# Optimization experiments

Measured on AMD Instinct MI355X. Metric: run time of the kernel, lower is better.

## Reference

```python
import jax, jax.numpy as jnp
import numpy as np

B, L, D, H = 8, 2048, 1024, 16
FACTOR = 3


def setup_inputs() -> dict:
    key = jax.random.key(0)
    ks = jax.random.split(key, 11)
    s = 0.02
    mk = lambda k, shp: jax.random.normal(k, shp, dtype=jnp.float32)
    return {
        "queries": mk(ks[0], (B, L, D)),
        "keys": mk(ks[1], (B, L, D)),
        "values": mk(ks[2], (B, L, D)),
        "Wq": mk(ks[3], (D, D)) * s, "bq": jnp.zeros((D,), jnp.float32),
        "Wk": mk(ks[4], (D, D)) * s, "bk": jnp.zeros((D,), jnp.float32),
        "Wv": mk(ks[5], (D, D)) * s, "bv": jnp.zeros((D,), jnp.float32),
        "Wo": mk(ks[6], (D, D)) * s, "bo": jnp.zeros((D,), jnp.float32),
    }


def reference(queries, keys, values, Wq, bq, Wk, bk, Wv, bv, Wo, bo):
    b, length, d = queries.shape
    h = H
    e = d // h
    q = (queries @ Wq + bq).reshape(b, length, h, e)
    k = (keys @ Wk + bk).reshape(b, length, h, e)
    v = (values @ Wv + bv).reshape(b, length, h, e)

    # [B, H, E, L] layout for FFT along time
    qf = jnp.fft.rfft(q.transpose(0, 2, 3, 1), axis=-1)
    kf = jnp.fft.rfft(k.transpose(0, 2, 3, 1), axis=-1)
    corr = jnp.fft.irfft(qf * jnp.conj(kf), n=length, axis=-1)  # [B,H,E,L]

    vperm = v.transpose(0, 2, 3, 1)  # [B,H,E,L]
    top_k = int(FACTOR * np.log(length))  # static: 22 for L=2048
    weights, delay = jax.lax.top_k(corr, top_k)          # [B,H,E,K]
    temp_corr = jax.nn.softmax(weights, axis=-1)         # [B,H,E,K]

    idx0 = jnp.arange(length)  # [L]
    agg = jnp.zeros_like(vperm)
    # small fixed loop over top-k delays (mirrors original structure)
    for i in range(top_k):
        # faithful to source: indices wrapped mod 8 (original code quirk)
        td = (idx0[None, None, None, :] + delay[..., i:i + 1]) % 8  # [B,H,E,L]
        pattern = jnp.take_along_axis(vperm, td, axis=-1)
        agg = agg + pattern * temp_corr[..., i:i + 1]

    result = agg.transpose(0, 3, 1, 2).reshape(b, length, d)  # [B,L,D]
    out = result @ Wo + bo
    return (out, corr.transpose(0, 3, 1, 2))
```

## Files before the change

kernel.cpp:

```cpp
#include <hip/hip_runtime.h>
#include <cstdint>
#include <cstddef>


#define TOPK 22

typedef __attribute__((ext_vector_type(8))) short short8;
typedef __attribute__((ext_vector_type(4))) float f32x4;

__device__ __forceinline__ float bf2f(unsigned short u) {
  union { unsigned int i; float f; } w;
  w.i = ((unsigned int)u) << 16;
  return w.f;
}
__device__ __forceinline__ unsigned short f2bf(float f) {
  union { float f; unsigned int i; } w;
  w.f = f;
  unsigned int x = w.i;
  x += 0x7fffu + ((x >> 16) & 1u);
  return (unsigned short)(x >> 16);
}

__device__ __forceinline__ float2 make2(float x, float y) { float2 r; r.x = x; r.y = y; return r; }
__device__ __forceinline__ float2 cadd(float2 a, float2 b) { return make2(a.x + b.x, a.y + b.y); }
__device__ __forceinline__ float2 csub(float2 a, float2 b) { return make2(a.x - b.x, a.y - b.y); }
__device__ __forceinline__ float2 cmul(float2 a, float2 b) {
  return make2(a.x * b.x - a.y * b.y, a.x * b.y + a.y * b.x);
}

__device__ __forceinline__ int cfi(int u) { return 2 * u + (((u) >> 5) << 1); }

template <bool INV>
__device__ __forceinline__ void dft8(float2 (&v)[8]) {
  const float C = 0.70710678118654752f;
  float2 s0 = cadd(v[0], v[4]), s1 = csub(v[0], v[4]);
  float2 s2 = cadd(v[2], v[6]), s3 = csub(v[2], v[6]);
  float2 E0 = cadd(s0, s2), E2 = csub(s0, s2);
  float2 E1, E3;
  if (!INV) { E1 = make2(s1.x + s3.y, s1.y - s3.x); E3 = make2(s1.x - s3.y, s1.y + s3.x); }
  else      { E1 = make2(s1.x - s3.y, s1.y + s3.x); E3 = make2(s1.x + s3.y, s1.y - s3.x); }
  float2 q0 = cadd(v[1], v[5]), q1 = csub(v[1], v[5]);
  float2 q2 = cadd(v[3], v[7]), q3 = csub(v[3], v[7]);
  float2 O0 = cadd(q0, q2), O2 = csub(q0, q2);
  float2 O1, O3;
  if (!INV) { O1 = make2(q1.x + q3.y, q1.y - q3.x); O3 = make2(q1.x - q3.y, q1.y + q3.x); }
  else      { O1 = make2(q1.x - q3.y, q1.y + q3.x); O3 = make2(q1.x + q3.y, q1.y - q3.x); }
  float2 T0 = O0, T1, T2, T3;
  if (!INV) {
    T1 = make2(C * (O1.x + O1.y), C * (O1.y - O1.x));
    T2 = make2(O2.y, -O2.x);
    T3 = make2(C * (O3.y - O3.x), -C * (O3.x + O3.y));
  } else {
    T1 = make2(C * (O1.x - O1.y), C * (O1.x + O1.y));
    T2 = make2(-O2.y, O2.x);
    T3 = make2(-C * (O3.x + O3.y), C * (O3.x - O3.y));
  }
  v[0] = cadd(E0, T0); v[4] = csub(E0, T0);
  v[1] = cadd(E1, T1); v[5] = csub(E1, T1);
  v[2] = cadd(E2, T2); v[6] = csub(E2, T2);
  v[3] = cadd(E3, T3); v[7] = csub(E3, T3);
}

template <bool INV>
__device__ __forceinline__ void dft4(float2 (&v)[4]) {
  float2 s0 = cadd(v[0], v[2]), s1 = csub(v[0], v[2]);
  float2 s2 = cadd(v[1], v[3]), s3 = csub(v[1], v[3]);
  v[0] = cadd(s0, s2); v[2] = csub(s0, s2);
  if (!INV) { v[1] = make2(s1.x + s3.y, s1.y - s3.x); v[3] = make2(s1.x - s3.y, s1.y + s3.x); }
  else      { v[1] = make2(s1.x - s3.y, s1.y + s3.x); v[3] = make2(s1.x + s3.y, s1.y - s3.x); }
}

template <int NS, bool INV>
__device__ __forceinline__ void stage8(const float* __restrict__ src,
                                       float* __restrict__ dst, int tid) {
  float2 v[8];
#pragma unroll
  for (int m = 0; m < 8; ++m)
    v[m] = *reinterpret_cast<const float2*>(src + cfi(tid + (m << 8)));
  if constexpr (NS > 1) {
    const int r = tid & (NS - 1);
    const float rev = (INV ? (1.0f / (8 * NS)) : (-1.0f / (8 * NS))) * (float)r;
    float2 w1; w1.x = __builtin_amdgcn_cosf(rev); w1.y = __builtin_amdgcn_sinf(rev);
    const float2 w2 = cmul(w1, w1);
    const float2 w3 = cmul(w2, w1);
    const float2 w4 = cmul(w2, w2);
    const float2 w5 = cmul(w4, w1);
    const float2 w6 = cmul(w4, w2);
    const float2 w7 = cmul(w4, w3);
    v[1] = cmul(v[1], w1); v[2] = cmul(v[2], w2); v[3] = cmul(v[3], w3);
    v[4] = cmul(v[4], w4); v[5] = cmul(v[5], w5); v[6] = cmul(v[6], w6);
    v[7] = cmul(v[7], w7);
  }
  dft8<INV>(v);
  const int r2 = tid & (NS - 1);
  const int d = ((tid & ~(NS - 1)) << 3) | r2;
#pragma unroll
  for (int m = 0; m < 8; ++m)
    *reinterpret_cast<float2*>(dst + cfi(d + m * NS)) = v[m];
}

__global__ __launch_bounds__(256) void transpose_w(
    const float* __restrict__ Wq, const float* __restrict__ Wk,
    unsigned short* __restrict__ WqT, unsigned short* __restrict__ WkT) {
  __shared__ unsigned short T[64][72];
  const float* src = blockIdx.z ? Wk : Wq;
  unsigned short* dst = blockIdx.z ? WkT : WqT;
  const int k0 = blockIdx.x * 64;
  const int n0 = blockIdx.y * 64;
  const int c = threadIdx.x & 63;
  const int r0 = threadIdx.x >> 6;
#pragma unroll
  for (int p = 0; p < 16; ++p) {
    const int r = r0 + 4 * p;
    T[c][r] = f2bf(src[(size_t)(k0 + r) * 1024 + n0 + c]);
  }
  __syncthreads();
#pragma unroll
  for (int p = 0; p < 16; ++p) {
    const int nn = r0 + 4 * p;
    dst[(size_t)(n0 + nn) * 1024 + k0 + c] = T[nn][c];
  }
}

__global__ __launch_bounds__(256, 2) void gemm_qk(
    const float* __restrict__ A,
    const unsigned short* __restrict__ WT,
    const float* __restrict__ bias,
    unsigned short* __restrict__ outT) {
  __shared__ __align__(16) unsigned short smem[16384];
  unsigned short* As = smem;
  unsigned short* Bs = smem + 4096;

  const int tid = threadIdx.x;
  const int lane = tid & 63;
  const int w = tid >> 6;
  const int wr = w >> 1, wc = w & 1;
  const int m0 = blockIdx.x * 128;
  const int n0 = blockIdx.y * 128;
  const int l15 = lane & 15;
  const int quad = lane >> 4;

  f32x4 acc[4][4];
#pragma unroll
  for (int i = 0; i < 4; ++i)
#pragma unroll
    for (int j = 0; j < 4; ++j)
#pragma unroll
      for (int r = 0; r < 4; ++r) acc[i][j][r] = 0.f;

  for (int k0 = 0; k0 < 1024; k0 += 32) {
    __syncthreads();
#pragma unroll
    for (int h = 0; h < 2; ++h) {
      const int c = tid + h * 256;
      const int row = c >> 2;
      const int kc = (c & 3) * 8;
      const float* ap = A + (size_t)(m0 + row) * 1024 + k0 + kc;
      const float4 a0 = *reinterpret_cast<const float4*>(ap);
      const float4 a1 = *reinterpret_cast<const float4*>(ap + 4);
      uint4 pa;
      pa.x = f2bf(a0.x) | ((unsigned int)f2bf(a0.y) << 16);
      pa.y = f2bf(a0.z) | ((unsigned int)f2bf(a0.w) << 16);
      pa.z = f2bf(a1.x) | ((unsigned int)f2bf(a1.y) << 16);
      pa.w = f2bf(a1.z) | ((unsigned int)f2bf(a1.w) << 16);
      *reinterpret_cast<uint4*>(As + row * 32 + kc) = pa;
      uint4 vb = *reinterpret_cast<const uint4*>(WT + (size_t)(n0 + row) * 1024 + k0 + kc);
      *reinterpret_cast<uint4*>(Bs + row * 32 + kc) = vb;
    }
    __syncthreads();

    short8 af[4], bfr[4];
#pragma unroll
    for (int mt = 0; mt < 4; ++mt)
      af[mt] = *reinterpret_cast<const short8*>(As + (wr * 64 + mt * 16 + l15) * 32 + quad * 8);
#pragma unroll
    for (int nt = 0; nt < 4; ++nt)
      bfr[nt] = *reinterpret_cast<const short8*>(Bs + (wc * 64 + nt * 16 + l15) * 32 + quad * 8);
#pragma unroll
    for (int mt = 0; mt < 4; ++mt)
#pragma unroll
      for (int nt = 0; nt < 4; ++nt)
        acc[mt][nt] = __builtin_amdgcn_mfma_f32_16x16x32_bf16(af[mt], bfr[nt], acc[mt][nt], 0, 0, 0);
  }

  __syncthreads();
  unsigned short* Cs = smem;
#pragma unroll
  for (int nt = 0; nt < 4; ++nt) {
    const int n_local = wc * 64 + nt * 16 + l15;
    const float bv = bias[n0 + n_local];
#pragma unroll
    for (int mt = 0; mt < 4; ++mt) {
      const int mbase = wr * 64 + mt * 16 + quad * 4;
#pragma unroll
      for (int r = 0; r < 4; ++r)
        Cs[n_local * 128 + mbase + r] = f2bf(acc[mt][nt][r] + bv);
    }
  }
  __syncthreads();

  const int b = m0 >> 11;
  const int l0 = m0 & 2047;
  for (int it = tid; it < 2048; it += 256) {
    const int rowi = it >> 4;
    const int ci = it & 15;
    uint4 v = *reinterpret_cast<const uint4*>(Cs + rowi * 128 + ci * 8);
    *reinterpret_cast<uint4*>(outT + (size_t)(b * 1024 + n0 + rowi) * 2048 + l0 + ci * 8) = v;
  }
}

__global__ __launch_bounds__(256) void vsmall_kernel(
    const float* __restrict__ values,
    const float* __restrict__ Wv,
    const float* __restrict__ bv,
    float* __restrict__ out) {
  __shared__ float xr[1024];
  const int m = blockIdx.x;
  const int b = m >> 3, t = m & 7;
  const float* row = values + ((size_t)b * 2048 + t) * 1024;
  for (int i = threadIdx.x; i < 1024; i += 256) xr[i] = row[i];
  __syncthreads();
  const int n = blockIdx.y * 256 + threadIdx.x;
  float acc = 0.f;
#pragma unroll 8
  for (int k = 0; k < 1024; ++k) acc += xr[k] * Wv[(size_t)k * 1024 + n];
  out[(size_t)m * 1024 + n] = acc + bv[n];
}

__global__ __launch_bounds__(256, 4) void corr_topk(
    const unsigned short* __restrict__ Qt,
    const unsigned short* Kt,
    const float* __restrict__ vsmall,
    unsigned short* corrOut,
    float* __restrict__ agg) {
  __shared__ __align__(16) float bufA[4224];
  __shared__ __align__(16) float bufB[4224];
  __shared__ float wtv[4][TOPK];
  __shared__ int   wti[4][TOPK];
  __shared__ float sel_val[TOPK];
  __shared__ int   sel_idx[TOPK];
  __shared__ float wsum[8];

  const int tid = threadIdx.x;
  const int lane = tid & 63;
  const int wv = tid >> 6;
  const int s = blockIdx.x;
  const size_t base = (size_t)s * 2048;

  {
    float2 v[8];
#pragma unroll
    for (int m = 0; m < 8; ++m) {
      const int u = tid + (m << 8);
      v[m] = make2(bf2f(Qt[base + u]), bf2f(Kt[base + u]));
    }
    dft8<false>(v);
    const int d = tid << 3;
#pragma unroll
    for (int m = 0; m < 8; ++m)
      *reinterpret_cast<float2*>(bufA + cfi(d + m)) = v[m];
  }
  __syncthreads();

  stage8<8, false>(bufA, bufB, tid);
  __syncthreads();
  stage8<64, false>(bufB, bufA, tid);
  __syncthreads();

  {
#pragma unroll
    for (int h = 0; h < 2; ++h) {
      const int j = tid + (h << 8);
      float2 v[4];
#pragma unroll
      for (int m = 0; m < 4; ++m)
        v[m] = *reinterpret_cast<const float2*>(bufA + cfi(j + (m << 9)));
      const float rev = -(1.0f / 2048.0f) * (float)j;
      float2 w1; w1.x = __builtin_amdgcn_cosf(rev); w1.y = __builtin_amdgcn_sinf(rev);
      const float2 w2 = cmul(w1, w1);
      const float2 w3 = cmul(w2, w1);
      v[1] = cmul(v[1], w1); v[2] = cmul(v[2], w2); v[3] = cmul(v[3], w3);
      dft4<false>(v);
#pragma unroll
      for (int m = 0; m < 4; ++m)
        *reinterpret_cast<float2*>(bufB + cfi(j + (m << 9))) = v[m];
    }
  }
  __syncthreads();

  {
    float2 v[8];
    const float ks = 1.0f / 8192.0f;
#pragma unroll
    for (int m = 0; m < 8; ++m) {
      const int u = tid + (m << 8);
      const int ub = (2048 - u) & 2047;
      const float2 Av = *reinterpret_cast<const float2*>(bufB + cfi(u));
      const float2 Bv = *reinterpret_cast<const float2*>(bufB + cfi(ub));
      const float Px = Av.x + Bv.x, Py = Av.y - Bv.y;
      const float Qx = Av.x - Bv.x, Qy = -Av.y - Bv.y;
      const float X1 = (Px * Qx - Py * Qy) * ks;
      const float Y1 = (Px * Qy + Py * Qx) * ks;
      v[m] = make2(-Y1, X1);
    }
    dft8<true>(v);
    const int d = tid << 3;
#pragma unroll
    for (int m = 0; m < 8; ++m)
      *reinterpret_cast<float2*>(bufA + cfi(d + m)) = v[m];
  }
  __syncthreads();

  stage8<8, true>(bufA, bufB, tid);
  __syncthreads();
  stage8<64, true>(bufB, bufA, tid);
  __syncthreads();

  float cval[8];
#pragma unroll
  for (int h = 0; h < 2; ++h) {
    const int j = tid + (h << 8);
    float2 v0 = *reinterpret_cast<const float2*>(bufA + cfi(j));
    float2 v1 = *reinterpret_cast<const float2*>(bufA + cfi(j + 512));
    float2 v2 = *reinterpret_cast<const float2*>(bufA + cfi(j + 1024));
    float2 v3 = *reinterpret_cast<const float2*>(bufA + cfi(j + 1536));
    const float rev = (1.0f / 2048.0f) * (float)j;
    float2 w1; w1.x = __builtin_amdgcn_cosf(rev); w1.y = __builtin_amdgcn_sinf(rev);
    const float2 w2 = cmul(w1, w1);
    const float2 w3 = cmul(w2, w1);
    const float2 t1 = cmul(v1, w1);
    const float2 t3 = cmul(v3, w3);
    const float t2x = v2.x * w2.x - v2.y * w2.y;
    cval[h]     = v0.x + t1.x + t2x + t3.x;
    cval[h + 2] = v0.x - t1.y - t2x + t3.y;
    cval[h + 4] = v0.x - t1.x + t2x - t3.x;
    cval[h + 6] = v0.x + t1.y - t2x - t3.y;
  }

#pragma unroll
  for (int i = 0; i < 8; ++i)
    corrOut[base + (size_t)(tid + (i << 8))] = f2bf(cval[i]);

  for (int r = 0; r < TOPK; ++r) {
    float bv = cval[0];
    int bi = tid;
#pragma unroll
    for (int i = 1; i < 8; ++i) {
      if (cval[i] > bv) { bv = cval[i]; bi = tid + (i << 8); }
    }
    for (int off = 32; off > 0; off >>= 1) {
      const float ov = __shfl_down(bv, off);
      const int oi = __shfl_down(bi, off);
      if (ov > bv || (ov == bv && oi < bi)) { bv = ov; bi = oi; }
    }
    const int bw = __shfl(bi, 0);
    if (lane == 0) { wtv[wv][r] = bv; wti[wv][r] = bi; }
#pragma unroll
    for (int i = 0; i < 8; ++i)
      if (bw == tid + (i << 8)) cval[i] = -3.4e38f;
  }
  __syncthreads();

  if (tid == 0) {
    int p0 = 0, p1 = 0, p2 = 0, p3 = 0;
    for (int r = 0; r < TOPK; ++r) {
      float bv = wtv[0][p0]; int bi = wti[0][p0]; int bwv = 0;
      float v1 = wtv[1][p1]; int i1 = wti[1][p1];
      if (v1 > bv || (v1 == bv && i1 < bi)) { bv = v1; bi = i1; bwv = 1; }
      float v2 = wtv[2][p2]; int i2 = wti[2][p2];
      if (v2 > bv || (v2 == bv && i2 < bi)) { bv = v2; bi = i2; bwv = 2; }
      float v3 = wtv[3][p3]; int i3 = wti[3][p3];
      if (v3 > bv || (v3 == bv && i3 < bi)) { bv = v3; bi = i3; bwv = 3; }
      sel_val[r] = bv; sel_idx[r] = bi;
      if (bwv == 0) ++p0; else if (bwv == 1) ++p1; else if (bwv == 2) ++p2; else ++p3;
    }
    const float m = sel_val[0];
    for (int c = 0; c < 8; ++c) wsum[c] = 0.f;
    float ssum = 0.f;
    for (int r = 0; r < TOPK; ++r) {
      const float e = __expf(sel_val[r] - m);
      ssum += e;
      wsum[sel_idx[r] & 7] += e;
    }
    const float inv = 1.f / ssum;
    for (int c = 0; c < 8; ++c) wsum[c] *= inv;
  }
  __syncthreads();

  if (tid < 8) {
    const int b = s >> 10, n = s & 1023;
    float a = 0.f;
#pragma unroll
    for (int c = 0; c < 8; ++c)
      a += wsum[c] * vsmall[(size_t)(b * 8 + ((tid + c) & 7)) * 1024 + n];
    agg[(size_t)(b * 8 + tid) * 1024 + n] = a;
  }
}

__global__ __launch_bounds__(256) void osmall_kernel(
    const float* __restrict__ aggin,
    const float* __restrict__ Wo,
    const float* __restrict__ bo,
    float* __restrict__ out) {
  __shared__ float xr[1024];
  const int m = blockIdx.x;
  const float* row = aggin + (size_t)m * 1024;
  for (int i = threadIdx.x; i < 1024; i += 256) xr[i] = row[i];
  __syncthreads();
  const int n = blockIdx.y * 256 + threadIdx.x;
  float acc = 0.f;
#pragma unroll 8
  for (int k = 0; k < 1024; ++k) acc += xr[k] * Wo[(size_t)k * 1024 + n];
  out[(size_t)m * 1024 + n] = acc + bo[n];
}

__global__ __launch_bounds__(256) void corr_transpose(
    const unsigned short* __restrict__ corrWs,
    float* __restrict__ out1) {
  __shared__ unsigned short T[64][72];
  const int bb = blockIdx.z;
  const int l0 = blockIdx.x * 64;
  const int n0 = blockIdx.y * 64;
  const int c = threadIdx.x & 63;
  const int r0 = threadIdx.x >> 6;
#pragma unroll
  for (int p = 0; p < 16; ++p) {
    const int r = r0 + 4 * p;
    T[c][r] = corrWs[(size_t)(bb * 1024 + n0 + r) * 2048 + l0 + c];
  }
  __syncthreads();
#pragma unroll
  for (int p = 0; p < 16; ++p) {
    const int ll = r0 + 4 * p;
    out1[(size_t)(bb * 2048 + l0 + ll) * 1024 + n0 + c] = bf2f(T[ll][c]);
  }
}

__global__ __launch_bounds__(256) void bcast_out(
    const float* __restrict__ outSmall,
    float* __restrict__ out0) {
  const size_t i4 = (size_t)blockIdx.x * 256 + threadIdx.x;
  const size_t basee = i4 * 4;
  const int n = (int)(basee & 1023);
  const int l = (int)((basee >> 10) & 2047);
  const int b = (int)(basee >> 21);
  const float4 v = *reinterpret_cast<const float4*>(outSmall + ((size_t)(b * 8 + (l & 7)) << 10) + n);
  *reinterpret_cast<float4*>(out0 + basee) = v;
}

extern "C" void kernel_launch(void* const* d_in, const int* in_sizes, int n_in,
                              void* d_out, int out_size, void* d_ws, size_t ws_size,
                              hipStream_t stream) {
  const float* queries = (const float*)d_in[0];
  const float* keys    = (const float*)d_in[1];
  const float* values  = (const float*)d_in[2];
  const float* Wq = (const float*)d_in[3];
  const float* bq = (const float*)d_in[4];
  const float* Wk = (const float*)d_in[5];
  const float* bk = (const float*)d_in[6];
  const float* Wv = (const float*)d_in[7];
  const float* bv = (const float*)d_in[8];
  const float* Wo = (const float*)d_in[9];
  const float* bo = (const float*)d_in[10];

  char* ws = (char*)d_ws;
  unsigned short* WqT = (unsigned short*)(ws);
  unsigned short* WkT = (unsigned short*)(ws + (2u << 20));
  unsigned short* Qt  = (unsigned short*)(ws + (4u << 20));
  float* vsmall   = (float*)(ws + (36u << 20));
  float* aggbuf   = (float*)(ws + (36u << 20) + (256u << 10));
  float* outSmall = (float*)(ws + (36u << 20) + (512u << 10));

  float* out0 = (float*)d_out;
  float* out1 = out0 + (size_t)16777216;
  unsigned short* Kt = (unsigned short*)d_out;
  unsigned short* corrWs = Kt;

  transpose_w<<<dim3(16, 16, 2), 256, 0, stream>>>(Wq, Wk, WqT, WkT);
  gemm_qk<<<dim3(128, 8), 256, 0, stream>>>(queries, WqT, bq, Qt);
  gemm_qk<<<dim3(128, 8), 256, 0, stream>>>(keys, WkT, bk, Kt);
  vsmall_kernel<<<dim3(64, 4), 256, 0, stream>>>(values, Wv, bv, vsmall);
  corr_topk<<<8192, 256, 0, stream>>>(Qt, Kt, vsmall, corrWs, aggbuf);
  osmall_kernel<<<dim3(64, 4), 256, 0, stream>>>(aggbuf, Wo, bo, outSmall);
  corr_transpose<<<dim3(32, 16, 8), 256, 0, stream>>>(corrWs, out1);
  bcast_out<<<16384, 256, 0, stream>>>(outSmall, out0);
}
```

Baseline: 744.3 us.

## Replace iterative top-k with radix-select threshold in corr_topk kernel

Replaces the 22-round per-wave argmax selection and serial single-thread merge with a 4-pass shared-memory radix select over order-preserving float keys. This finds the exact 22nd-largest threshold, then resolves ties by lowest index. Softmax weights are accumulated by atomics into 8 bins keyed by index mod 8, and the result is normalized at the end. This removes many shuffle reductions and a serial tail, at the cost of more block-wide barriers and shared atomics.

```diff
diff --git a/kernel.cpp b/kernel.cpp
--- a/kernel.cpp
+++ b/kernel.cpp
@@ -99,6 +99,36 @@
     *reinterpret_cast<float2*>(dst + cfi(d + m * NS)) = v[m];
 }
 
+__device__ __forceinline__ void radix_pick(const unsigned int* h,
+                                           unsigned int* sb,
+                                           unsigned int need, int tid) {
+  if (tid < 64) {
+    const unsigned int c0 = h[4 * tid + 0];
+    const unsigned int c1 = h[4 * tid + 1];
+    const unsigned int c2 = h[4 * tid + 2];
+    const unsigned int c3 = h[4 * tid + 3];
+    const unsigned int g = c0 + c1 + c2 + c3;
+    unsigned int S = g;
+#pragma unroll
+    for (int off = 1; off < 64; off <<= 1) {
+      const unsigned int o = __shfl_down(S, off);
+      if (tid + off < 64) S += o;
+    }
+    unsigned int A = S - g;
+    int pick = -1;
+    unsigned int nn = 0;
+    const unsigned int cc[4] = {c0, c1, c2, c3};
+#pragma unroll
+    for (int j = 3; j >= 0; --j) {
+      if (pick < 0) {
+        if (A < need && need <= A + cc[j]) { pick = j; nn = need - A; }
+        else A += cc[j];
+      }
+    }
+    if (pick >= 0) { sb[0] = (unsigned int)(4 * tid + pick); sb[1] = nn; }
+  }
+}
+
 __global__ __launch_bounds__(256) void transpose_w(
     const float* __restrict__ Wq, const float* __restrict__ Wk,
     unsigned short* __restrict__ WqT, unsigned short* __restrict__ WkT) {
@@ -235,17 +265,18 @@
     float* __restrict__ agg) {
   __shared__ __align__(16) float bufA[4224];
   __shared__ __align__(16) float bufB[4224];
-  __shared__ float wtv[4][TOPK];
-  __shared__ int   wti[4][TOPK];
-  __shared__ float sel_val[TOPK];
-  __shared__ int   sel_idx[TOPK];
-  __shared__ float wsum[8];
 
   const int tid = threadIdx.x;
   const int lane = tid & 63;
   const int wv = tid >> 6;
   const int s = blockIdx.x;
   const size_t base = (size_t)s * 2048;
+
+  unsigned int* hist = reinterpret_cast<unsigned int*>(bufB);
+  float* bins = bufB + 1024;
+  float* wred = bufB + 1032;
+  int* ired = reinterpret_cast<int*>(bufB + 1036);
+  unsigned int* sb = reinterpret_cast<unsigned int*>(bufB + 1040);
 
   {
     float2 v[8];
@@ -341,59 +372,101 @@
   for (int i = 0; i < 8; ++i)
     corrOut[base + (size_t)(tid + (i << 8))] = f2bf(cval[i]);
 
-  for (int r = 0; r < TOPK; ++r) {
-    float bv = cval[0];
-    int bi = tid;
-#pragma unroll
-    for (int i = 1; i < 8; ++i) {
-      if (cval[i] > bv) { bv = cval[i]; bi = tid + (i << 8); }
-    }
+  unsigned int key[8];
+#pragma unroll
+  for (int i = 0; i < 8; ++i) {
+    union { float f; unsigned int u; } cvt;
+    cvt.f = cval[i];
+    const unsigned int b = cvt.u;
+    key[i] = (b & 0x80000000u) ? ~b : (b | 0x80000000u);
+  }
+
+#pragma unroll
+  for (int q = 0; q < 4; ++q) hist[(q << 8) + tid] = 0u;
+  if (tid < 8) bins[tid] = 0.f;
+  {
+    float vm = cval[0];
+#pragma unroll
+    for (int i = 1; i < 8; ++i) vm = fmaxf(vm, cval[i]);
+#pragma unroll
+    for (int off = 32; off > 0; off >>= 1) vm = fmaxf(vm, __shfl_down(vm, off));
+    if (lane == 0) wred[wv] = vm;
+  }
+  __syncthreads();
+  const float mx = fmaxf(fmaxf(wred[0], wred[1]), fmaxf(wred[2], wred[3]));
+
+  unsigned int prefix = 0;
+  unsigned int need = TOPK;
+#pragma unroll
+  for (int i = 0; i < 8; ++i) atomicAdd(&hist[key[i] >> 24], 1u);
+  __syncthreads();
+  radix_pick(hist, sb, need, tid);
+  __syncthreads();
+  prefix = sb[0]; need = sb[1];
+#pragma unroll
+  for (int i = 0; i < 8; ++i)
+    if ((key[i] >> 24) == prefix) atomicAdd(&hist[256 + ((key[i] >> 16) & 255u)], 1u);
+  __syncthreads();
+  radix_pick(hist + 256, sb, need, tid);
+  __syncthreads();
+  prefix = (prefix << 8) | sb[0]; need = sb[1];
+#pragma unroll
+  for (int i = 0; i < 8; ++i)
+    if ((key[i] >> 16) == prefix) atomicAdd(&hist[512 + ((key[i] >> 8) & 255u)], 1u);
+  __syncthreads();
+  radix_pick(hist + 512, sb, need, tid);
+  __syncthreads();
+  prefix = (prefix << 8) | sb[0]; need = sb[1];
+#pragma unroll
+  for (int i = 0; i < 8; ++i)
+    if ((key[i] >> 8) == prefix) atomicAdd(&hist[768 + (key[i] & 255u)], 1u);
+  __syncthreads();
+  radix_pick(hist + 768, sb, need, tid);
+  __syncthreads();
+  const unsigned int T = (prefix << 8) | sb[0];
+  const unsigned int takeEq = sb[1];
+
+  unsigned int eqm = 0, selEq = 0;
+#pragma unroll
+  for (int i = 0; i < 8; ++i)
+    if (key[i] == T) eqm |= (1u << i);
+  for (unsigned int it2 = 0; it2 < takeEq; ++it2) {
+    int mi = 0x7fffffff;
+#pragma unroll
+    for (int i = 0; i < 8; ++i)
+      if (eqm & (1u << i)) mi = min(mi, tid + (i << 8));
+#pragma unroll
     for (int off = 32; off > 0; off >>= 1) {
-      const float ov = __shfl_down(bv, off);
-      const int oi = __shfl_down(bi, off);
-      if (ov > bv || (ov == bv && oi < bi)) { bv = ov; bi = oi; }
-    }
-    const int bw = __shfl(bi, 0);
-    if (lane == 0) { wtv[wv][r] = bv; wti[wv][r] = bi; }
+      const int o = __shfl_down(mi, off);
+      if (lane + off < 64) mi = min(mi, o);
+    }
+    if (lane == 0) ired[wv] = mi;
+    __syncthreads();
+    const int gm = min(min(ired[0], ired[1]), min(ired[2], ired[3]));
 #pragma unroll
     for (int i = 0; i < 8; ++i)
-      if (bw == tid + (i << 8)) cval[i] = -3.4e38f;
-  }
-  __syncthreads();
-
-  if (tid == 0) {
-    int p0 = 0, p1 = 0, p2 = 0, p3 = 0;
-    for (int r = 0; r < TOPK; ++r) {
-      float bv = wtv[0][p0]; int bi = wti[0][p0]; int bwv = 0;
-      float v1 = wtv[1][p1]; int i1 = wti[1][p1];
-      if (v1 > bv || (v1 == bv && i1 < bi)) { bv = v1; bi = i1; bwv = 1; }
-      float v2 = wtv[2][p2]; int i2 = wti[2][p2];
-      if (v2 > bv || (v2 == bv && i2 < bi)) { bv = v2; bi = i2; bwv = 2; }
-      float v3 = wtv[3][p3]; int i3 = wti[3][p3];
-      if (v3 > bv || (v3 == bv && i3 < bi)) { bv = v3; bi = i3; bwv = 3; }
-      sel_val[r] = bv; sel_idx[r] = bi;
-      if (bwv == 0) ++p0; else if (bwv == 1) ++p1; else if (bwv == 2) ++p2; else ++p3;
-    }
-    const float m = sel_val[0];
-    for (int c = 0; c < 8; ++c) wsum[c] = 0.f;
-    float ssum = 0.f;
-    for (int r = 0; r < TOPK; ++r) {
-      const float e = __expf(sel_val[r] - m);
-      ssum += e;
-      wsum[sel_idx[r] & 7] += e;
-    }
-    const float inv = 1.f / ssum;
-    for (int c = 0; c < 8; ++c) wsum[c] *= inv;
-  }
+      if ((tid + (i << 8)) == gm) { selEq |= (1u << i); eqm &= ~(1u << i); }
+    if (it2 + 1 < takeEq) __syncthreads();
+  }
+
+  float esum = 0.f;
+#pragma unroll
+  for (int i = 0; i < 8; ++i) {
+    const bool sel = (key[i] > T) || ((selEq >> i) & 1u);
+    if (sel) esum += __expf(cval[i] - mx);
+  }
+  if (esum > 0.f) atomicAdd(&bins[tid & 7], esum);
   __syncthreads();
 
   if (tid < 8) {
+    const float ssum = bins[0] + bins[1] + bins[2] + bins[3] +
+                       bins[4] + bins[5] + bins[6] + bins[7];
     const int b = s >> 10, n = s & 1023;
     float a = 0.f;
 #pragma unroll
     for (int c = 0; c < 8; ++c)
-      a += wsum[c] * vsmall[(size_t)(b * 8 + ((tid + c) & 7)) * 1024 + n];
-    agg[(size_t)(b * 8 + tid) * 1024 + n] = a;
+      a += bins[c] * vsmall[(size_t)(b * 8 + ((tid + c) & 7)) * 1024 + n];
+    agg[(size_t)(b * 8 + tid) * 1024 + n] = a / ssum;
   }
 }
 
```

Measured after the change: 611.5 us. 17.9% less time.
